# Kernel tuning notes

Hardware: AMD Instinct MI355X
Metric: run time of the kernel (lower is better)

Reference implementation:

```python
import jax, jax.numpy as jnp
import numpy as np

N = 100000
E = 1600000
EPS = 1e-5
NEG_SLOPE = 0.01


def _leaky(x):
    return jnp.where(x > 0, x, NEG_SLOPE * x)


def _conv2d(x, w, b):
    # x: [N,Cin,H,W], w: [Cout,Cin,kh,kw], VALID padding, stride 1
    y = jax.lax.conv_general_dilated(x, w, (1, 1), 'VALID',
                                     dimension_numbers=('NCHW', 'OIHW', 'NCHW'))
    return y + b[None, :, None, None]


def _bn(x, g, b, m, v):
    # eval-mode BatchNorm1d over feature dim
    return (x - m) * (g / jnp.sqrt(v + EPS)) + b


def setup_inputs() -> dict:
    key = jax.random.key(0)
    ks = jax.random.split(key, 64)
    d = {}
    d['inputs'] = jax.random.normal(ks[0], (N, 1, 100, 5), dtype=jnp.float32)
    d['edge_index'] = jax.random.randint(ks[1], (2, E), 0, N, dtype=jnp.int32)
    # CNN encoder params (x=10)
    d['cw1'] = 0.1 * jax.random.normal(ks[2], (10, 1, 3, 3), dtype=jnp.float32)
    d['cb1'] = jnp.zeros((10,), jnp.float32)
    d['cw2'] = 0.1 * jax.random.normal(ks[3], (20, 10, 3, 2), dtype=jnp.float32)
    d['cb2'] = jnp.zeros((20,), jnp.float32)
    d['cw3'] = 0.1 * jax.random.normal(ks[4], (1, 20, 3, 2), dtype=jnp.float32)
    d['cb3'] = jnp.zeros((1,), jnp.float32)
    dims = [94, 128, 128, 64, 64, 16]
    for i in range(5):
        fi, fo = dims[i], dims[i + 1]
        k = 8 + 4 * i
        d[f'gw{i+1}'] = jax.random.normal(ks[k], (fi, fo), jnp.float32) / np.sqrt(fi)
        d[f'gb{i+1}'] = jnp.zeros((fo,), jnp.float32)
        d[f'bn{i+1}_g'] = 1.0 + 0.1 * jax.random.normal(ks[k + 1], (fo,), jnp.float32)
        d[f'bn{i+1}_b'] = 0.1 * jax.random.normal(ks[k + 2], (fo,), jnp.float32)
        d[f'bn{i+1}_m'] = 0.1 * jax.random.normal(ks[k + 3], (fo,), jnp.float32)
        d[f'bn{i+1}_v'] = jax.random.uniform(ks[k + 3], (fo,), jnp.float32, 0.5, 1.5)
    return d


def reference(inputs, edge_index,
              cw1, cb1, cw2, cb2, cw3, cb3,
              gw1, gb1, gw2, gb2, gw3, gb3, gw4, gb4, gw5, gb5,
              bn1_g, bn1_b, bn1_m, bn1_v,
              bn2_g, bn2_b, bn2_m, bn2_v,
              bn3_g, bn3_b, bn3_m, bn3_v,
              bn4_g, bn4_b, bn4_m, bn4_v,
              bn5_g, bn5_b, bn5_m, bn5_v):
    n = inputs.shape[0]
    # --- GCN normalization (self-loops + symmetric deg^-1/2) ---
    loops = jnp.arange(n, dtype=edge_index.dtype)
    src = jnp.concatenate([edge_index[0], loops])
    dst = jnp.concatenate([edge_index[1], loops])
    deg = jax.ops.segment_sum(jnp.ones_like(src, dtype=jnp.float32), dst, num_segments=n)
    dinv = jnp.where(deg > 0, jax.lax.rsqrt(deg), 0.0)
    norm = dinv[src] * dinv[dst]  # [E+N]

    def gcn(h, w, b):
        m = (h @ w)[src] * norm[:, None]
        return jax.ops.segment_sum(m, dst, num_segments=n) + b

    # --- CNN encoder (dropout identity in eval) ---
    h = _conv2d(inputs, cw1, cb1)
    h = _leaky(h)
    h = _conv2d(h, cw2, cb2)
    h = _leaky(h)
    h = _conv2d(h, cw3, cb3)  # [N,1,94,1]
    h = jnp.tanh(h.reshape(-1, 94))

    h = jnp.tanh(_bn(gcn(h, gw1, gb1), bn1_g, bn1_b, bn1_m, bn1_v))
    h = jnp.tanh(_bn(gcn(h, gw2, gb2), bn2_g, bn2_b, bn2_m, bn2_v))
    h = jnp.tanh(_bn(gcn(h, gw3, gb3), bn3_g, bn3_b, bn3_m, bn3_v))
    h = jnp.tanh(_bn(gcn(h, gw4, gb4), bn4_g, bn4_b, bn4_m, bn4_v))
    h = _bn(gcn(h, gw5, gb5), bn5_g, bn5_b, bn5_m, bn5_v)
    return jax.nn.softmax(h, axis=1)
```

## Files before the change

kernel.cpp:

```cpp
#include <hip/hip_runtime.h>
#include <math.h>

namespace {

constexpr int NN = 100000;
constexpr int NE = 1600000;
constexpr float EPS = 1e-5f;

__device__ __forceinline__ float leaky(float x) { return fmaxf(x, 0.01f * x); }
__device__ __forceinline__ float ffma(float a, float b, float c) { return __builtin_fmaf(a, b, c); }


__global__ __launch_bounds__(256) void k_init(int* __restrict__ deg, int* __restrict__ counter, int n) {
  int i = blockIdx.x * 256 + threadIdx.x;
  if (i < n) deg[i] = 1;
  if (i == 0) counter[0] = 0;
}

__global__ __launch_bounds__(256) void k_count(const int* __restrict__ dst, int* __restrict__ deg, int e) {
  int i = blockIdx.x * 256 + threadIdx.x;
  if (i < e) atomicAdd(&deg[dst[i]], 1);
}

__global__ __launch_bounds__(256) void k_alloc(const int* __restrict__ deg, float* __restrict__ dinv,
                                               int* __restrict__ offsets, int* __restrict__ cursor,
                                               int* __restrict__ counter, int n) {
  int i = blockIdx.x * 256 + threadIdx.x;
  int lane = threadIdx.x & 63;
  int c = 0;
  if (i < n) {
    int d = deg[i];
    dinv[i] = rsqrtf((float)d);
    c = d - 1;
  }
  int v = c;
#pragma unroll
  for (int s = 1; s < 64; s <<= 1) {
    int t = __shfl_up(v, s, 64);
    if (lane >= s) v += t;
  }
  int total = __shfl(v, 63, 64);
  int base = 0;
  if (lane == 63) base = atomicAdd(counter, total);
  base = __shfl(base, 63, 64);
  if (i < n) {
    int off = base + v - c;
    offsets[i] = off;
    cursor[i] = off;
  }
}

__global__ __launch_bounds__(256) void k_fill(const int* __restrict__ src, const int* __restrict__ dst,
                                              const float* __restrict__ dinv, int* __restrict__ cursor,
                                              int* __restrict__ adj_src, float* __restrict__ adj_norm, int e) {
  int i = blockIdx.x * 256 + threadIdx.x;
  if (i < e) {
    int s = src[i], d = dst[i];
    int p = atomicAdd(&cursor[d], 1);
    adj_src[p] = s;
    adj_norm[p] = dinv[s] * dinv[d];
  }
}

__global__ __launch_bounds__(256) void k_padw1(const float* __restrict__ gw1, float* __restrict__ w1p) {
  int i = blockIdx.x * 256 + threadIdx.x;
  if (i < 96 * 128) w1p[i] = (i < 94 * 128) ? gw1[i] : 0.f;
}

__global__ __launch_bounds__(256, 4) void k_cnn(const float* __restrict__ x,
                                             const float* __restrict__ cw1, const float* __restrict__ cb1,
                                             const float* __restrict__ cw2, const float* __restrict__ cb2,
                                             const float* __restrict__ cw3, const float* __restrict__ cb3,
                                             float* __restrict__ H) {
  __shared__ __align__(16) float inb[2][500];
  __shared__ float c1[2][2940];
  __shared__ float part[2][2][2][98];

  int tid = threadIdx.x;
  int half = tid >> 7;
  int nt = tid & 127;
  int lane = tid & 63;
  int node = blockIdx.x * 2 + half;
  int co0 = __builtin_amdgcn_readfirstlane(((tid >> 6) & 1) * 10);

  for (int i = tid; i < 2 * 2 * 2 * 98; i += 256) ((float*)part)[i] = 0.f;

  if (nt < 125) {
    const float4* xp = (const float4*)(x + (size_t)node * 500);
    ((float4*)inb[half])[nt] = xp[nt];
  }
  __syncthreads();

  {
    const float* in = inb[half];
    float* c1p = c1[half];
    int h = nt;
    if (h < 98) {
      float xv[3][5];
#pragma unroll
      for (int kh = 0; kh < 3; kh++)
#pragma unroll
        for (int c = 0; c < 5; c++) xv[kh][c] = in[(h + kh) * 5 + c];
      float* rowp = c1p + h * 3;
#pragma unroll
      for (int co = 0; co < 10; co++) {
        float b = cb1[co];
        float a0 = b, a1 = b, a2 = b;
#pragma unroll
        for (int kh = 0; kh < 3; kh++)
#pragma unroll
          for (int kw = 0; kw < 3; kw++) {
            float wv = cw1[co * 9 + kh * 3 + kw];
            a0 = ffma(xv[kh][kw + 0], wv, a0);
            a1 = ffma(xv[kh][kw + 1], wv, a1);
            a2 = ffma(xv[kh][kw + 2], wv, a2);
          }
        rowp[co * 294 + 0] = leaky(a0);
        rowp[co * 294 + 1] = leaky(a1);
        rowp[co * 294 + 2] = leaky(a2);
      }
    }
  }
  __syncthreads();

  int hg = lane >> 1, w = lane & 1;
  int h0 = hg * 3;
  float acc[3][10];
#pragma unroll
  for (int a = 0; a < 3; a++)
#pragma unroll
    for (int c = 0; c < 10; c++) acc[a][c] = 0.f;
  {
    const float* c1p = c1[half];
#pragma unroll 1
    for (int ci = 0; ci < 10; ci++) {
      float r[5][2];
      const float* base = c1p + ci * 294 + h0 * 3 + w;
#pragma unroll
      for (int i = 0; i < 5; i++) {
        r[i][0] = base[i * 3];
        r[i][1] = base[i * 3 + 1];
      }
#pragma unroll
      for (int c = 0; c < 10; c++) {
        const float* wp = cw2 + (co0 + c) * 60 + ci * 6;
        float w0 = wp[0], w1 = wp[1], w2v = wp[2], w3v = wp[3], w4 = wp[4], w5 = wp[5];
#pragma unroll
        for (int hh = 0; hh < 3; hh++) {
          float t = acc[hh][c];
          t = ffma(r[hh][0],     w0,  t);
          t = ffma(r[hh][1],     w1,  t);
          t = ffma(r[hh + 1][0], w2v, t);
          t = ffma(r[hh + 1][1], w3v, t);
          t = ffma(r[hh + 2][0], w4,  t);
          t = ffma(r[hh + 2][1], w5,  t);
          acc[hh][c] = t;
        }
      }
    }
#pragma unroll
    for (int c = 0; c < 10; c++) {
      float b = cb2[co0 + c];
#pragma unroll
      for (int hh = 0; hh < 3; hh++) acc[hh][c] = leaky(acc[hh][c] + b);
    }
  }
  __syncthreads();

  {
    float* pp = &part[half][co0 == 0 ? 0 : 1][w][0];
#pragma unroll
    for (int kh = 0; kh < 3; kh++) {
      float ws[10];
#pragma unroll
      for (int c = 0; c < 10; c++) {
        float wa = cw3[(co0 + c) * 6 + kh * 2 + 0];
        float wb = cw3[(co0 + c) * 6 + kh * 2 + 1];
        ws[c] = w ? wb : wa;
      }
#pragma unroll
      for (int hh = 0; hh < 3; hh++) {
        float s = 0.f;
#pragma unroll
        for (int c = 0; c < 10; c++) s = ffma(acc[hh][c], ws[c], s);
        pp[h0 + hh - kh + 2] += s;
      }
      __syncthreads();
    }
  }

  {
    float* Hp = H + (size_t)node * 96;
    if (nt < 94) {
      float v = part[half][0][0][nt + 2] + part[half][0][1][nt + 2]
              + part[half][1][0][nt + 2] + part[half][1][1][nt + 2] + cb3[0];
      Hp[nt] = tanhf(v);
    } else if (nt < 96) {
      Hp[nt] = 0.f;
    }
  }
}

template <int K, int FO, int BN>
__global__ __launch_bounds__(256) void k_gemm(const float* __restrict__ A, const float* __restrict__ W,
                                              float* __restrict__ C, int M) {
  __shared__ float As[64][K + 1];
  __shared__ __align__(16) float Ws[K][BN];
  int tid = threadIdx.x;
  int row_base = blockIdx.x * 64;
  int col_base = blockIdx.y * BN;

  for (int idx = tid; idx < 64 * K; idx += 256) {
    int r = idx / K, k = idx - r * K;
    int row = row_base + r;
    As[r][k] = (row < M) ? A[(size_t)row * K + k] : 0.f;
  }
  for (int idx = tid; idx < K * BN; idx += 256) {
    int r = idx / BN, c = idx - r * BN;
    Ws[r][c] = W[r * FO + col_base + c];
  }
  __syncthreads();

  if constexpr (BN == 64) {
    int ty = tid >> 4, tx = tid & 15;
    float acc[4][4] = {};
#pragma unroll 4
    for (int k = 0; k < K; k++) {
      float a0 = As[ty * 4 + 0][k];
      float a1 = As[ty * 4 + 1][k];
      float a2 = As[ty * 4 + 2][k];
      float a3 = As[ty * 4 + 3][k];
      const float4 b = *(const float4*)&Ws[k][tx * 4];
      acc[0][0] = ffma(a0, b.x, acc[0][0]); acc[0][1] = ffma(a0, b.y, acc[0][1]);
      acc[0][2] = ffma(a0, b.z, acc[0][2]); acc[0][3] = ffma(a0, b.w, acc[0][3]);
      acc[1][0] = ffma(a1, b.x, acc[1][0]); acc[1][1] = ffma(a1, b.y, acc[1][1]);
      acc[1][2] = ffma(a1, b.z, acc[1][2]); acc[1][3] = ffma(a1, b.w, acc[1][3]);
      acc[2][0] = ffma(a2, b.x, acc[2][0]); acc[2][1] = ffma(a2, b.y, acc[2][1]);
      acc[2][2] = ffma(a2, b.z, acc[2][2]); acc[2][3] = ffma(a2, b.w, acc[2][3]);
      acc[3][0] = ffma(a3, b.x, acc[3][0]); acc[3][1] = ffma(a3, b.y, acc[3][1]);
      acc[3][2] = ffma(a3, b.z, acc[3][2]); acc[3][3] = ffma(a3, b.w, acc[3][3]);
    }
#pragma unroll
    for (int i = 0; i < 4; i++) {
      int row = row_base + ty * 4 + i;
      if (row < M) {
        float4 v = make_float4(acc[i][0], acc[i][1], acc[i][2], acc[i][3]);
        *(float4*)&C[(size_t)row * FO + col_base + tx * 4] = v;
      }
    }
  } else {
    int ty = tid >> 2, tx = tid & 3;
    float acc[4] = {};
#pragma unroll 4
    for (int k = 0; k < K; k++) {
      float a = As[ty][k];
      const float4 b = *(const float4*)&Ws[k][tx * 4];
      acc[0] = ffma(a, b.x, acc[0]); acc[1] = ffma(a, b.y, acc[1]);
      acc[2] = ffma(a, b.z, acc[2]); acc[3] = ffma(a, b.w, acc[3]);
    }
    int row = row_base + ty;
    if (row < M) *(float4*)&C[(size_t)row * FO + col_base + tx * 4] = make_float4(acc[0], acc[1], acc[2], acc[3]);
  }
}

template <int FO, bool SOFT>
__global__ __launch_bounds__(256) void k_agg(const float* __restrict__ XW,
                                             const int* __restrict__ offsets, const int* __restrict__ deg,
                                             const int* __restrict__ adj_src, const float* __restrict__ adj_norm,
                                             const float* __restrict__ dinv,
                                             const float* __restrict__ gb, const float* __restrict__ bg,
                                             const float* __restrict__ bb, const float* __restrict__ bm,
                                             const float* __restrict__ bv,
                                             float* __restrict__ out, int n) {
  constexpr int TPN = FO / 4;
  constexpr int NPB = 256 / TPN;
  int tid = threadIdx.x;
  int li = tid / TPN, c4 = (tid % TPN) * 4;
  int node = blockIdx.x * NPB + li;
  if (node >= n) return;

  float dv = dinv[node];
  float se = dv * dv;
  float4 acc = *(const float4*)&XW[(size_t)node * FO + c4];
  acc.x *= se; acc.y *= se; acc.z *= se; acc.w *= se;
  int start = offsets[node];
  int cnt = deg[node] - 1;
  for (int e = 0; e < cnt; e++) {
    int s = adj_src[start + e];
    float nm = adj_norm[start + e];
    float4 v = *(const float4*)&XW[(size_t)s * FO + c4];
    acc.x = ffma(v.x, nm, acc.x);
    acc.y = ffma(v.y, nm, acc.y);
    acc.z = ffma(v.z, nm, acc.z);
    acc.w = ffma(v.w, nm, acc.w);
  }
  const float4 g4 = *(const float4*)&bg[c4];
  const float4 v4 = *(const float4*)&bv[c4];
  const float4 gb4 = *(const float4*)&gb[c4];
  const float4 bm4 = *(const float4*)&bm[c4];
  const float4 bb4 = *(const float4*)&bb[c4];
  float4 r;
  r.x = ffma(acc.x + gb4.x - bm4.x, g4.x * rsqrtf(v4.x + EPS), bb4.x);
  r.y = ffma(acc.y + gb4.y - bm4.y, g4.y * rsqrtf(v4.y + EPS), bb4.y);
  r.z = ffma(acc.z + gb4.z - bm4.z, g4.z * rsqrtf(v4.z + EPS), bb4.z);
  r.w = ffma(acc.w + gb4.w - bm4.w, g4.w * rsqrtf(v4.w + EPS), bb4.w);
  if constexpr (SOFT) {
    float mx = fmaxf(fmaxf(r.x, r.y), fmaxf(r.z, r.w));
#pragma unroll
    for (int m = TPN / 2; m; m >>= 1) mx = fmaxf(mx, __shfl_xor(mx, m, TPN));
    r.x = expf(r.x - mx); r.y = expf(r.y - mx);
    r.z = expf(r.z - mx); r.w = expf(r.w - mx);
    float sm = r.x + r.y + r.z + r.w;
#pragma unroll
    for (int m = TPN / 2; m; m >>= 1) sm += __shfl_xor(sm, m, TPN);
    float inv = 1.f / sm;
    r.x *= inv; r.y *= inv; r.z *= inv; r.w *= inv;
  } else {
    r.x = tanhf(r.x); r.y = tanhf(r.y); r.z = tanhf(r.z); r.w = tanhf(r.w);
  }
  *(float4*)&out[(size_t)node * FO + c4] = r;
}

}

extern "C" void kernel_launch(void* const* d_in, const int* in_sizes, int n_in,
                              void* d_out, int out_size, void* d_ws, size_t ws_size,
                              hipStream_t stream) {
  const float* x   = (const float*)d_in[0];
  const int*   ei  = (const int*)d_in[1];
  const float* cw1 = (const float*)d_in[2];
  const float* cb1 = (const float*)d_in[3];
  const float* cw2 = (const float*)d_in[4];
  const float* cb2 = (const float*)d_in[5];
  const float* cw3 = (const float*)d_in[6];
  const float* cb3 = (const float*)d_in[7];
  const float *gw[5], *gb[5], *bng[5], *bnb[5], *bnm[5], *bnv[5];
  for (int l = 0; l < 5; l++) {
    gw[l]  = (const float*)d_in[8 + 6 * l + 0];
    gb[l]  = (const float*)d_in[8 + 6 * l + 1];
    bng[l] = (const float*)d_in[8 + 6 * l + 2];
    bnb[l] = (const float*)d_in[8 + 6 * l + 3];
    bnm[l] = (const float*)d_in[8 + 6 * l + 4];
    bnv[l] = (const float*)d_in[8 + 6 * l + 5];
  }
  const int* srcp = ei;
  const int* dstp = ei + NE;

  char* w = (char*)d_ws;
  auto alloc = [&](size_t bytes) { char* p = w; w += (bytes + 255) & ~255ULL; return p; };
  int*   deg     = (int*)alloc((size_t)NN * 4);
  int*   offsets = (int*)alloc((size_t)NN * 4);
  int*   cursor  = (int*)alloc((size_t)NN * 4);
  int*   counter = (int*)alloc(256);
  float* dinv    = (float*)alloc((size_t)NN * 4);
  int*   adj_src = (int*)alloc((size_t)NE * 4);
  float* adj_nm  = (float*)alloc((size_t)NE * 4);
  float* w1p     = (float*)alloc(96 * 128 * 4);
  float* bufA    = (float*)alloc((size_t)NN * 128 * 4);
  float* bufB    = (float*)alloc((size_t)NN * 128 * 4);
  float* bufC    = (float*)alloc((size_t)NN * 128 * 4);

  int nb_n = (NN + 255) / 256;
  int nb_e = (NE + 255) / 256;
  k_init<<<nb_n, 256, 0, stream>>>(deg, counter, NN);
  k_count<<<nb_e, 256, 0, stream>>>(dstp, deg, NE);
  k_alloc<<<nb_n, 256, 0, stream>>>(deg, dinv, offsets, cursor, counter, NN);
  k_fill<<<nb_e, 256, 0, stream>>>(srcp, dstp, dinv, cursor, adj_src, adj_nm, NE);
  k_padw1<<<48, 256, 0, stream>>>(gw[0], w1p);

  k_cnn<<<NN / 2, 256, 0, stream>>>(x, cw1, cb1, cw2, cb2, cw3, cb3, bufA);

  int gx = (NN + 63) / 64;
  k_gemm<96, 128, 64><<<dim3(gx, 2), 256, 0, stream>>>(bufA, w1p, bufB, NN);
  k_agg<128, false><<<(NN + 7) / 8, 256, 0, stream>>>(bufB, offsets, deg, adj_src, adj_nm, dinv,
                                                      gb[0], bng[0], bnb[0], bnm[0], bnv[0], bufC, NN);
  k_gemm<128, 128, 64><<<dim3(gx, 2), 256, 0, stream>>>(bufC, gw[1], bufB, NN);
  k_agg<128, false><<<(NN + 7) / 8, 256, 0, stream>>>(bufB, offsets, deg, adj_src, adj_nm, dinv,
                                                      gb[1], bng[1], bnb[1], bnm[1], bnv[1], bufA, NN);
  k_gemm<128, 64, 64><<<dim3(gx, 1), 256, 0, stream>>>(bufA, gw[2], bufB, NN);
  k_agg<64, false><<<(NN + 15) / 16, 256, 0, stream>>>(bufB, offsets, deg, adj_src, adj_nm, dinv,
                                                       gb[2], bng[2], bnb[2], bnm[2], bnv[2], bufC, NN);
  k_gemm<64, 64, 64><<<dim3(gx, 1), 256, 0, stream>>>(bufC, gw[3], bufB, NN);
  k_agg<64, false><<<(NN + 15) / 16, 256, 0, stream>>>(bufB, offsets, deg, adj_src, adj_nm, dinv,
                                                       gb[3], bng[3], bnb[3], bnm[3], bnv[3], bufA, NN);
  k_gemm<64, 16, 16><<<dim3(gx, 1), 256, 0, stream>>>(bufA, gw[4], bufB, NN);
  k_agg<16, true><<<(NN + 63) / 64, 256, 0, stream>>>(bufB, offsets, deg, adj_src, adj_nm, dinv,
                                                      gb[4], bng[4], bnb[4], bnm[4], bnv[4], (float*)d_out, NN);
}
```

Measured before the change: 1.489 ms.

## Pack adjacency as int2, widen aggregation to 8 features/thread, precompute BN affine

Stores the CSR source index and edge norm together as one int2 array, so each edge needs one 8-byte load instead of two separate loads. The aggregation kernel now has each thread handle 8 features (two float4s) and processes two edges per loop iteration, which raises memory-level parallelism per thread. Batch-norm scale and shift for all five layers are precomputed once in a small kernel, and grid sizes are adjusted to match. Each edge's metadata is now loaded by half as many threads per node, at the cost of more registers and half as many threads per node.

```diff
diff --git a/kernel.cpp b/kernel.cpp
--- a/kernel.cpp
+++ b/kernel.cpp
@@ -52,19 +52,37 @@
 
 __global__ __launch_bounds__(256) void k_fill(const int* __restrict__ src, const int* __restrict__ dst,
                                               const float* __restrict__ dinv, int* __restrict__ cursor,
-                                              int* __restrict__ adj_src, float* __restrict__ adj_norm, int e) {
+                                              int2* __restrict__ adj, int e) {
   int i = blockIdx.x * 256 + threadIdx.x;
   if (i < e) {
     int s = src[i], d = dst[i];
     int p = atomicAdd(&cursor[d], 1);
-    adj_src[p] = s;
-    adj_norm[p] = dinv[s] * dinv[d];
+    adj[p] = make_int2(s, __float_as_int(dinv[s] * dinv[d]));
   }
 }
 
 __global__ __launch_bounds__(256) void k_padw1(const float* __restrict__ gw1, float* __restrict__ w1p) {
   int i = blockIdx.x * 256 + threadIdx.x;
   if (i < 96 * 128) w1p[i] = (i < 94 * 128) ? gw1[i] : 0.f;
+}
+
+struct BNParams {
+  const float* bg[5];
+  const float* bv[5];
+  const float* gb[5];
+  const float* bm[5];
+  const float* bb[5];
+};
+__global__ __launch_bounds__(512) void k_bnprep(BNParams p, float* __restrict__ scale, float* __restrict__ shift) {
+  int i = threadIdx.x;
+  if (i >= 400) return;
+  const int ends[5] = {128, 256, 320, 384, 400};
+  int l = 0;
+  while (i >= ends[l]) l++;
+  int c = i - (l ? ends[l - 1] : 0);
+  float sc = p.bg[l][c] * rsqrtf(p.bv[l][c] + EPS);
+  scale[i] = sc;
+  shift[i] = ffma(p.gb[l][c] - p.bm[l][c], sc, p.bb[l][c]);
 }
 
 __global__ __launch_bounds__(256, 4) void k_cnn(const float* __restrict__ x,
@@ -266,59 +284,88 @@
 template <int FO, bool SOFT>
 __global__ __launch_bounds__(256) void k_agg(const float* __restrict__ XW,
                                              const int* __restrict__ offsets, const int* __restrict__ deg,
-                                             const int* __restrict__ adj_src, const float* __restrict__ adj_norm,
+                                             const int2* __restrict__ adj,
                                              const float* __restrict__ dinv,
-                                             const float* __restrict__ gb, const float* __restrict__ bg,
-                                             const float* __restrict__ bb, const float* __restrict__ bm,
-                                             const float* __restrict__ bv,
-                                             float* __restrict__ out, int n) {
-  constexpr int TPN = FO / 4;
+                                             const float* __restrict__ bnscale, const float* __restrict__ bnshift,
+                                             int bnofs, float* __restrict__ out, int n) {
+  constexpr int TPN = FO / 8;
   constexpr int NPB = 256 / TPN;
   int tid = threadIdx.x;
-  int li = tid / TPN, c4 = (tid % TPN) * 4;
+  int li = tid / TPN, c8 = (tid % TPN) * 8;
   int node = blockIdx.x * NPB + li;
   if (node >= n) return;
 
   float dv = dinv[node];
   float se = dv * dv;
-  float4 acc = *(const float4*)&XW[(size_t)node * FO + c4];
-  acc.x *= se; acc.y *= se; acc.z *= se; acc.w *= se;
-  int start = offsets[node];
+  const float4* selfp = (const float4*)&XW[(size_t)node * FO + c8];
+  float4 aL = selfp[0], aH = selfp[1];
+  aL.x *= se; aL.y *= se; aL.z *= se; aL.w *= se;
+  aH.x *= se; aH.y *= se; aH.z *= se; aH.w *= se;
+
+  const int2* ap = adj + offsets[node];
   int cnt = deg[node] - 1;
-  for (int e = 0; e < cnt; e++) {
-    int s = adj_src[start + e];
-    float nm = adj_norm[start + e];
-    float4 v = *(const float4*)&XW[(size_t)s * FO + c4];
-    acc.x = ffma(v.x, nm, acc.x);
-    acc.y = ffma(v.y, nm, acc.y);
-    acc.z = ffma(v.z, nm, acc.z);
-    acc.w = ffma(v.w, nm, acc.w);
-  }
-  const float4 g4 = *(const float4*)&bg[c4];
-  const float4 v4 = *(const float4*)&bv[c4];
-  const float4 gb4 = *(const float4*)&gb[c4];
-  const float4 bm4 = *(const float4*)&bm[c4];
-  const float4 bb4 = *(const float4*)&bb[c4];
-  float4 r;
-  r.x = ffma(acc.x + gb4.x - bm4.x, g4.x * rsqrtf(v4.x + EPS), bb4.x);
-  r.y = ffma(acc.y + gb4.y - bm4.y, g4.y * rsqrtf(v4.y + EPS), bb4.y);
-  r.z = ffma(acc.z + gb4.z - bm4.z, g4.z * rsqrtf(v4.z + EPS), bb4.z);
-  r.w = ffma(acc.w + gb4.w - bm4.w, g4.w * rsqrtf(v4.w + EPS), bb4.w);
+  int e = 0;
+  for (; e + 1 < cnt; e += 2) {
+    int2 a0 = ap[e], a1 = ap[e + 1];
+    float nm0 = __int_as_float(a0.y), nm1 = __int_as_float(a1.y);
+    const float4* q0 = (const float4*)&XW[(size_t)a0.x * FO + c8];
+    const float4* q1 = (const float4*)&XW[(size_t)a1.x * FO + c8];
+    float4 v0 = q0[0], w0 = q0[1];
+    float4 v1 = q1[0], w1 = q1[1];
+    aL.x = ffma(v0.x, nm0, aL.x); aL.y = ffma(v0.y, nm0, aL.y);
+    aL.z = ffma(v0.z, nm0, aL.z); aL.w = ffma(v0.w, nm0, aL.w);
+    aH.x = ffma(w0.x, nm0, aH.x); aH.y = ffma(w0.y, nm0, aH.y);
+    aH.z = ffma(w0.z, nm0, aH.z); aH.w = ffma(w0.w, nm0, aH.w);
+    aL.x = ffma(v1.x, nm1, aL.x); aL.y = ffma(v1.y, nm1, aL.y);
+    aL.z = ffma(v1.z, nm1, aL.z); aL.w = ffma(v1.w, nm1, aL.w);
+    aH.x = ffma(w1.x, nm1, aH.x); aH.y = ffma(w1.y, nm1, aH.y);
+    aH.z = ffma(w1.z, nm1, aH.z); aH.w = ffma(w1.w, nm1, aH.w);
+  }
+  if (e < cnt) {
+    int2 a0 = ap[e];
+    float nm0 = __int_as_float(a0.y);
+    const float4* q0 = (const float4*)&XW[(size_t)a0.x * FO + c8];
+    float4 v0 = q0[0], w0 = q0[1];
+    aL.x = ffma(v0.x, nm0, aL.x); aL.y = ffma(v0.y, nm0, aL.y);
+    aL.z = ffma(v0.z, nm0, aL.z); aL.w = ffma(v0.w, nm0, aL.w);
+    aH.x = ffma(w0.x, nm0, aH.x); aH.y = ffma(w0.y, nm0, aH.y);
+    aH.z = ffma(w0.z, nm0, aH.z); aH.w = ffma(w0.w, nm0, aH.w);
+  }
+
+  const float4 s4L = *(const float4*)&bnscale[bnofs + c8];
+  const float4 s4H = *(const float4*)&bnscale[bnofs + c8 + 4];
+  const float4 h4L = *(const float4*)&bnshift[bnofs + c8];
+  const float4 h4H = *(const float4*)&bnshift[bnofs + c8 + 4];
+  float r[8];
+  r[0] = ffma(aL.x, s4L.x, h4L.x); r[1] = ffma(aL.y, s4L.y, h4L.y);
+  r[2] = ffma(aL.z, s4L.z, h4L.z); r[3] = ffma(aL.w, s4L.w, h4L.w);
+  r[4] = ffma(aH.x, s4H.x, h4H.x); r[5] = ffma(aH.y, s4H.y, h4H.y);
+  r[6] = ffma(aH.z, s4H.z, h4H.z); r[7] = ffma(aH.w, s4H.w, h4H.w);
+
+  float4 oL, oH;
   if constexpr (SOFT) {
-    float mx = fmaxf(fmaxf(r.x, r.y), fmaxf(r.z, r.w));
+    float mx = r[0];
+#pragma unroll
+    for (int i = 1; i < 8; i++) mx = fmaxf(mx, r[i]);
 #pragma unroll
     for (int m = TPN / 2; m; m >>= 1) mx = fmaxf(mx, __shfl_xor(mx, m, TPN));
-    r.x = expf(r.x - mx); r.y = expf(r.y - mx);
-    r.z = expf(r.z - mx); r.w = expf(r.w - mx);
-    float sm = r.x + r.y + r.z + r.w;
+    float sm = 0.f;
+#pragma unroll
+    for (int i = 0; i < 8; i++) { r[i] = expf(r[i] - mx); sm += r[i]; }
 #pragma unroll
     for (int m = TPN / 2; m; m >>= 1) sm += __shfl_xor(sm, m, TPN);
     float inv = 1.f / sm;
-    r.x *= inv; r.y *= inv; r.z *= inv; r.w *= inv;
+#pragma unroll
+    for (int i = 0; i < 8; i++) r[i] *= inv;
   } else {
-    r.x = tanhf(r.x); r.y = tanhf(r.y); r.z = tanhf(r.z); r.w = tanhf(r.w);
-  }
-  *(float4*)&out[(size_t)node * FO + c4] = r;
+#pragma unroll
+    for (int i = 0; i < 8; i++) r[i] = tanhf(r[i]);
+  }
+  oL = make_float4(r[0], r[1], r[2], r[3]);
+  oH = make_float4(r[4], r[5], r[6], r[7]);
+  float4* op = (float4*)&out[(size_t)node * FO + c8];
+  op[0] = oL;
+  op[1] = oH;
 }
 
 }
@@ -353,9 +400,10 @@
   int*   cursor  = (int*)alloc((size_t)NN * 4);
   int*   counter = (int*)alloc(256);
   float* dinv    = (float*)alloc((size_t)NN * 4);
-  int*   adj_src = (int*)alloc((size_t)NE * 4);
-  float* adj_nm  = (float*)alloc((size_t)NE * 4);
+  int2*  adj     = (int2*)alloc((size_t)NE * 8);
   float* w1p     = (float*)alloc(96 * 128 * 4);
+  float* bnscale = (float*)alloc(400 * 4);
+  float* bnshift = (float*)alloc(400 * 4);
   float* bufA    = (float*)alloc((size_t)NN * 128 * 4);
   float* bufB    = (float*)alloc((size_t)NN * 128 * 4);
   float* bufC    = (float*)alloc((size_t)NN * 128 * 4);
@@ -365,25 +413,33 @@
   k_init<<<nb_n, 256, 0, stream>>>(deg, counter, NN);
   k_count<<<nb_e, 256, 0, stream>>>(dstp, deg, NE);
   k_alloc<<<nb_n, 256, 0, stream>>>(deg, dinv, offsets, cursor, counter, NN);
-  k_fill<<<nb_e, 256, 0, stream>>>(srcp, dstp, dinv, cursor, adj_src, adj_nm, NE);
+  k_fill<<<nb_e, 256, 0, stream>>>(srcp, dstp, dinv, cursor, adj, NE);
   k_padw1<<<48, 256, 0, stream>>>(gw[0], w1p);
+  {
+    BNParams bp;
+    for (int l = 0; l < 5; l++) {
+      bp.bg[l] = bng[l]; bp.bv[l] = bnv[l]; bp.gb[l] = gb[l];
+      bp.bm[l] = bnm[l]; bp.bb[l] = bnb[l];
+    }
+    k_bnprep<<<1, 512, 0, stream>>>(bp, bnscale, bnshift);
+  }
 
   k_cnn<<<NN / 2, 256, 0, stream>>>(x, cw1, cb1, cw2, cb2, cw3, cb3, bufA);
 
   int gx = (NN + 63) / 64;
   k_gemm<96, 128, 64><<<dim3(gx, 2), 256, 0, stream>>>(bufA, w1p, bufB, NN);
-  k_agg<128, false><<<(NN + 7) / 8, 256, 0, stream>>>(bufB, offsets, deg, adj_src, adj_nm, dinv,
-                                                      gb[0], bng[0], bnb[0], bnm[0], bnv[0], bufC, NN);
+  k_agg<128, false><<<(NN + 15) / 16, 256, 0, stream>>>(bufB, offsets, deg, adj, dinv,
+                                                        bnscale, bnshift, 0, bufC, NN);
   k_gemm<128, 128, 64><<<dim3(gx, 2), 256, 0, stream>>>(bufC, gw[1], bufB, NN);
-  k_agg<128, false><<<(NN + 7) / 8, 256, 0, stream>>>(bufB, offsets, deg, adj_src, adj_nm, dinv,
-                                                      gb[1], bng[1], bnb[1], bnm[1], bnv[1], bufA, NN);
+  k_agg<128, false><<<(NN + 15) / 16, 256, 0, stream>>>(bufB, offsets, deg, adj, dinv,
+                                                        bnscale, bnshift, 128, bufA, NN);
   k_gemm<128, 64, 64><<<dim3(gx, 1), 256, 0, stream>>>(bufA, gw[2], bufB, NN);
-  k_agg<64, false><<<(NN + 15) / 16, 256, 0, stream>>>(bufB, offsets, deg, adj_src, adj_nm, dinv,
-                                                       gb[2], bng[2], bnb[2], bnm[2], bnv[2], bufC, NN);
+  k_agg<64, false><<<(NN + 31) / 32, 256, 0, stream>>>(bufB, offsets, deg, adj, dinv,
+                                                       bnscale, bnshift, 256, bufC, NN);
   k_gemm<64, 64, 64><<<dim3(gx, 1), 256, 0, stream>>>(bufC, gw[3], bufB, NN);
-  k_agg<64, false><<<(NN + 15) / 16, 256, 0, stream>>>(bufB, offsets, deg, adj_src, adj_nm, dinv,
-                                                       gb[3], bng[3], bnb[3], bnm[3], bnv[3], bufA, NN);
+  k_agg<64, false><<<(NN + 31) / 32, 256, 0, stream>>>(bufB, offsets, deg, adj, dinv,
+                                                       bnscale, bnshift, 320, bufA, NN);
   k_gemm<64, 16, 16><<<dim3(gx, 1), 256, 0, stream>>>(bufA, gw[4], bufB, NN);
-  k_agg<16, true><<<(NN + 63) / 64, 256, 0, stream>>>(bufB, offsets, deg, adj_src, adj_nm, dinv,
-                                                      gb[4], bng[4], bnb[4], bnm[4], bnv[4], (float*)d_out, NN);
-}
+  k_agg<16, true><<<(NN + 127) / 128, 256, 0, stream>>>(bufB, offsets, deg, adj, dinv,
+                                                        bnscale, bnshift, 384, (float*)d_out, NN);
+}
```

After: 1.433 ms. -3.8%, faster.
